# Kernel optimization log

Hardware: AMD Instinct MI355X
Metric: run time of the kernel (lower is better)

## Reference

```python
import jax, jax.numpy as jnp
import numpy as np

N = 20000          # nodes
E = 320000         # edges (avg degree 16)
F_IN = 512         # in_channels
HID = 64           # hidden_channels
H1 = 8             # conv1 heads (hard-coded in source)
C_OUT = 7          # out_channels (num classes)
OUT2 = C_OUT * C_OUT  # conv2 per-head output dim = out_channels**2
H2 = 8             # conv2 heads
NC = 64            # number of clusters
NIDX = 10000       # |cluster_index|
NEG_SLOPE = 0.2    # PyG GATConv default leaky-relu slope


def gat_conv(x, edge_index, W, att_src, att_dst, bias, concat):
    """PyG GATConv (add_self_loops=True, eval mode so attention dropout is off)."""
    n = x.shape[0]
    H, C = att_src.shape
    h = (x @ W).reshape(n, H, C)                      # [n, H, C]
    loop = jnp.arange(n)
    src = jnp.concatenate([edge_index[0], loop])      # self loops appended
    dst = jnp.concatenate([edge_index[1], loop])
    a_src = jnp.einsum('nhc,hc->nh', h, att_src)      # [n, H]
    a_dst = jnp.einsum('nhc,hc->nh', h, att_dst)
    e = jax.nn.leaky_relu(a_src[src] + a_dst[dst], NEG_SLOPE)   # [Etot, H]
    # segment softmax over incoming edges of each destination node
    m = jax.lax.stop_gradient(jax.ops.segment_max(e, dst, num_segments=n))
    p = jnp.exp(e - m[dst])
    denom = jax.ops.segment_sum(p, dst, num_segments=n)
    alpha = p / denom[dst]                            # [Etot, H]
    out = jax.ops.segment_sum(alpha[:, :, None] * h[src], dst, num_segments=n)  # [n, H, C]
    if concat:
        return out.reshape(n, H * C) + bias
    return out.mean(axis=1) + bias


def setup_inputs() -> dict:
    key = jax.random.key(0)
    ks = jax.random.split(key, 12)
    s1 = 1.0 / np.sqrt(F_IN)
    s2 = 1.0 / np.sqrt(2 * HID * H1)
    return {
        'x': jax.random.normal(ks[0], (N, F_IN), dtype=jnp.float32),
        'edge_index': jax.random.randint(ks[1], (2, E), 0, N),
        'cluster_id': jax.random.uniform(ks[2], (N, NC), dtype=jnp.float32),
        'cluster_index': jax.random.randint(ks[3], (NIDX,), 0, N),
        'W1': jax.random.normal(ks[4], (F_IN, H1 * HID), dtype=jnp.float32) * s1,
        'att_src1': jax.random.normal(ks[5], (H1, HID), dtype=jnp.float32) * 0.1,
        'att_dst1': jax.random.normal(ks[6], (H1, HID), dtype=jnp.float32) * 0.1,
        'b1': jnp.zeros((H1 * HID,), dtype=jnp.float32),
        'W2': jax.random.normal(ks[7], (2 * H1 * HID, H2 * OUT2), dtype=jnp.float32) * s2,
        'att_src2': jax.random.normal(ks[8], (H2, OUT2), dtype=jnp.float32) * 0.1,
        'att_dst2': jax.random.normal(ks[9], (H2, OUT2), dtype=jnp.float32) * 0.1,
        'b2': jnp.zeros((OUT2,), dtype=jnp.float32),
    }


def reference(x, edge_index, cluster_id, cluster_index,
              W1, att_src1, att_dst1, b1, W2, att_src2, att_dst2, b2):
    n = x.shape[0]
    # eval mode: F.dropout and attention dropout are identity
    h = jax.nn.elu(gat_conv(x, edge_index, W1, att_src1, att_dst1, b1, concat=True))  # [N, H1*HID]
    cid = cluster_id[cluster_index]                       # [NIDX, NC]
    cluster_features = (cid.T @ h[cluster_index]) / cid.sum(0)[:, None]  # [NC, H1*HID]
    x1 = cluster_features[jnp.argmax(cluster_id, axis=1)] # [N, H1*HID]
    xx = jnp.concatenate([jnp.concatenate([h, x1], 1),
                          jnp.concatenate([x1, h], 1)], 0)  # [2N, 2*H1*HID]
    ei2 = jnp.concatenate([edge_index, edge_index + n], 1)  # doubled graph
    return gat_conv(xx, ei2, W2, att_src2, att_dst2, b2, concat=False)  # [2N, OUT2]
```

## Files before the change

### kernel.cpp

```cpp
#include <hip/hip_runtime.h>

#define NNODES 20000
#define NEDGES 320000
#define FIN    512
#define HC1    512
#define NHEAD  8
#define OUT2   49
#define NCOL2  392
#define NB2    784
#define NCLU   64
#define NIDX   10000
#define NEG    0.2f

typedef unsigned short u16;
typedef short bf16x8 __attribute__((ext_vector_type(8)));
typedef float f32x4 __attribute__((ext_vector_type(4)));

static __device__ __forceinline__ float lrelu(float v){ return v > 0.f ? v : NEG*v; }

static __device__ __forceinline__ u16 f2bf_hi(float f, float& rem) {
  union { float f; unsigned u; } c; c.f = f;
  unsigned hb = c.u & 0xFFFF0000u;
  union { unsigned u; float f; } d; d.u = hb;
  rem = f - d.f;
  return (u16)(hb >> 16);
}
static __device__ __forceinline__ u16 f2bf(float f) {
  union { float f; unsigned u; } c; c.f = f;
  return (u16)(c.u >> 16);
}
static __device__ __forceinline__ u16 f2bf_rn(float f) {
  union { float f; unsigned u; } c; c.f = f;
  unsigned r = c.u + 0x7FFFu + ((c.u >> 16) & 1u);
  return (u16)(r >> 16);
}
static __device__ __forceinline__ float bf2f(u16 u) {
  union { unsigned u; float f; } c; c.u = ((unsigned)u) << 16;
  return c.f;
}
static __device__ __forceinline__ void load8bf(const u16* p, float* o) {
  ushort4 a = *(const ushort4*)p;
  ushort4 b = *(const ushort4*)(p + 4);
  o[0]=bf2f(a.x); o[1]=bf2f(a.y); o[2]=bf2f(a.z); o[3]=bf2f(a.w);
  o[4]=bf2f(b.x); o[5]=bf2f(b.y); o[6]=bf2f(b.z); o[7]=bf2f(b.w);
}

__global__ void tw1_kernel(const float* __restrict__ W1, u16* __restrict__ Th, u16* __restrict__ Tl) {
  int idx = blockIdx.x*256 + threadIdx.x;
  int k = idx >> 9, j = idx & 511;
  float rem; u16 hi = f2bf_hi(W1[idx], rem);
  Th[(size_t)j*512 + k] = hi;
  Tl[(size_t)j*512 + k] = f2bf(rem);
}

__global__ void tb2_kernel(const float* __restrict__ W2, u16* __restrict__ Th, u16* __restrict__ Tl) {
  int idx = blockIdx.x*256 + threadIdx.x;
  int k = idx / NB2, j = idx - k*NB2;
  float v = (j < NCOL2) ? W2[(size_t)k*NCOL2 + j] : W2[(size_t)(512+k)*NCOL2 + (j - NCOL2)];
  float rem; u16 hi = f2bf_hi(v, rem);
  Th[(size_t)j*512 + k] = hi;
  Tl[(size_t)j*512 + k] = f2bf(rem);
}

template<int EPI>
__global__ __launch_bounds__(256) void gemm_mfma(
    const float* __restrict__ A,
    const u16* __restrict__ Bh, const u16* __restrict__ Bl,
    u16* __restrict__ Cbf, int M, int Ncols,
    const int* __restrict__ cmax, const float* __restrict__ CFW, u16* __restrict__ h2)
{
  __shared__ __align__(16) u16 As[2][128][40];
  __shared__ __align__(16) u16 Bs[2][128][40];
  int tid = threadIdx.x;
  int row0 = blockIdx.x * 128;
  int col0 = blockIdx.y * 128;
  int lane = tid & 63;
  int wid = tid >> 6;
  int wr = (wid >> 1) * 64;
  int wc = (wid & 1) * 64;
  int l16 = lane & 15;
  int q = lane >> 4;
  f32x4 acc[4][4];
  #pragma unroll
  for (int i = 0; i < 4; i++)
    #pragma unroll
    for (int j = 0; j < 4; j++)
      acc[i][j] = (f32x4){0.f, 0.f, 0.f, 0.f};

  int srow = tid >> 2;
  int sq = tid & 3;
  const uint4 z4 = make_uint4(0,0,0,0);

  for (int k0 = 0; k0 < 512; k0 += 32) {
    #pragma unroll
    for (int part = 0; part < 2; part++) {
      int r = part*64 + srow;
      int gm = row0 + r;
      float4 v0 = make_float4(0.f,0.f,0.f,0.f), v1 = v0;
      if (gm < M) {
        v0 = *(const float4*)(A + (size_t)gm*512 + k0 + sq*8);
        v1 = *(const float4*)(A + (size_t)gm*512 + k0 + sq*8 + 4);
      }
      float rem;
      ushort4 h0, l0, h1, l1;
      h0.x = f2bf_hi(v0.x, rem); l0.x = f2bf(rem);
      h0.y = f2bf_hi(v0.y, rem); l0.y = f2bf(rem);
      h0.z = f2bf_hi(v0.z, rem); l0.z = f2bf(rem);
      h0.w = f2bf_hi(v0.w, rem); l0.w = f2bf(rem);
      h1.x = f2bf_hi(v1.x, rem); l1.x = f2bf(rem);
      h1.y = f2bf_hi(v1.y, rem); l1.y = f2bf(rem);
      h1.z = f2bf_hi(v1.z, rem); l1.z = f2bf(rem);
      h1.w = f2bf_hi(v1.w, rem); l1.w = f2bf(rem);
      *(ushort4*)&As[0][r][sq*8]     = h0;
      *(ushort4*)&As[0][r][sq*8 + 4] = h1;
      *(ushort4*)&As[1][r][sq*8]     = l0;
      *(ushort4*)&As[1][r][sq*8 + 4] = l1;
      int gn = col0 + r;
      uint4 wh = z4, wl = z4;
      if (gn < Ncols) {
        wh = *(const uint4*)(Bh + (size_t)gn*512 + k0 + sq*8);
        wl = *(const uint4*)(Bl + (size_t)gn*512 + k0 + sq*8);
      }
      *(uint4*)&Bs[0][r][sq*8] = wh;
      *(uint4*)&Bs[1][r][sq*8] = wl;
    }
    __syncthreads();
    bf16x8 ah[4], al[4], bh[4], bl[4];
    #pragma unroll
    for (int i = 0; i < 4; i++) {
      ah[i] = *(const bf16x8*)&As[0][wr + i*16 + l16][q*8];
      al[i] = *(const bf16x8*)&As[1][wr + i*16 + l16][q*8];
      bh[i] = *(const bf16x8*)&Bs[0][wc + i*16 + l16][q*8];
      bl[i] = *(const bf16x8*)&Bs[1][wc + i*16 + l16][q*8];
    }
    #pragma unroll
    for (int i = 0; i < 4; i++)
      #pragma unroll
      for (int j = 0; j < 4; j++) {
        acc[i][j] = __builtin_amdgcn_mfma_f32_16x16x32_bf16(ah[i], bh[j], acc[i][j], 0, 0, 0);
        acc[i][j] = __builtin_amdgcn_mfma_f32_16x16x32_bf16(ah[i], bl[j], acc[i][j], 0, 0, 0);
        acc[i][j] = __builtin_amdgcn_mfma_f32_16x16x32_bf16(al[i], bh[j], acc[i][j], 0, 0, 0);
      }
    __syncthreads();
  }

  if (EPI == 0) {
    #pragma unroll
    for (int i = 0; i < 4; i++) {
      #pragma unroll
      for (int r = 0; r < 4; r++) {
        int m = row0 + wr + i*16 + q*4 + r;
        if (m < M) {
          #pragma unroll
          for (int j = 0; j < 4; j++)
            Cbf[(size_t)m*Ncols + col0 + wc + j*16 + l16] = f2bf_rn(acc[i][j][r]);
        }
      }
    }
  } else {
    #pragma unroll
    for (int i = 0; i < 4; i++) {
      #pragma unroll
      for (int r = 0; r < 4; r++) {
        int m = row0 + wr + i*16 + q*4 + r;
        if (m >= M) continue;
        int c = cmax[m];
        const float* cf = CFW + (size_t)c * NB2;
        #pragma unroll
        for (int j = 0; j < 4; j++) {
          int n = col0 + wc + j*16 + l16;
          if (n >= NB2) continue;
          float v = acc[i][j][r];
          if (n < NCOL2) h2[(size_t)m*NCOL2 + n] = f2bf_rn(v + cf[NCOL2 + n]);
          else           h2[(size_t)(NNODES + m)*NCOL2 + (n - NCOL2)] = f2bf_rn(v + cf[n - NCOL2]);
        }
      }
    }
  }
}

__global__ void hist_kernel(const int* __restrict__ ei, int* __restrict__ counts) {
  int e = blockIdx.x*256 + threadIdx.x;
  if (e < NEDGES) atomicAdd(&counts[ei[NEDGES + e]], 1);
}

__global__ __launch_bounds__(1024) void scan_kernel(const int* __restrict__ counts,
                                                    int* __restrict__ rowptr, int* __restrict__ cursor) {
  __shared__ int part[1024];
  int t = threadIdx.x;
  const int CH = 20;
  int start = t*CH;
  int end = min(start+CH, NNODES);
  int sum = 0;
  for (int i = start; i < end; i++) sum += counts[i];
  part[t] = sum;
  __syncthreads();
  for (int off = 1; off < 1024; off <<= 1) {
    int v = part[t];
    int add = (t >= off) ? part[t-off] : 0;
    __syncthreads();
    part[t] = v + add;
    __syncthreads();
  }
  int run = part[t] - sum;
  for (int i = start; i < end; i++) {
    rowptr[i] = run; cursor[i] = run;
    run += counts[i];
  }
  if (t == 1023) rowptr[NNODES] = part[1023];
}

__global__ void scatter_kernel(const int* __restrict__ ei, int* __restrict__ cursor, int* __restrict__ csr) {
  int e = blockIdx.x*256 + threadIdx.x;
  if (e < NEDGES) {
    int src = ei[e];
    int dst = ei[NEDGES + e];
    int pos = atomicAdd(&cursor[dst], 1);
    csr[pos] = src;
  }
}

__global__ __launch_bounds__(256) void a1_kernel(
    const u16* __restrict__ hpre, const float* __restrict__ atts, const float* __restrict__ attd,
    float* __restrict__ as1, float* __restrict__ ad1)
{
  int lane = threadIdx.x & 63;
  int i = blockIdx.x*4 + (threadIdx.x >> 6);
  float hv[8];
  load8bf(hpre + (size_t)i*HC1 + lane*8, hv);
  const float* ap = atts + lane*8; const float* dp = attd + lane*8;
  float ps = 0.f, pd = 0.f;
  #pragma unroll
  for (int k = 0; k < 8; k++) { ps = fmaf(hv[k], ap[k], ps); pd = fmaf(hv[k], dp[k], pd); }
  ps += __shfl_down(ps, 4, 8); ps += __shfl_down(ps, 2, 8); ps += __shfl_down(ps, 1, 8);
  pd += __shfl_down(pd, 4, 8); pd += __shfl_down(pd, 2, 8); pd += __shfl_down(pd, 1, 8);
  if ((lane & 7) == 0) {
    as1[i*8 + (lane >> 3)] = ps;
    ad1[i*8 + (lane >> 3)] = pd;
  }
}

__global__ __launch_bounds__(256) void softmax1_kernel(
    const float* __restrict__ as1, const float* __restrict__ ad1,
    const int* __restrict__ rp, const int* __restrict__ csr,
    float* __restrict__ p1, float* __restrict__ selfw, float* __restrict__ invs)
{
  int gid = blockIdx.x*256 + threadIdx.x;
  int i = gid >> 3, h = gid & 7;
  int rs = rp[i], re = rp[i+1];
  float adst = ad1[gid];
  float ps = __expf(lrelu(as1[gid] + adst));
  float s = ps;
  for (int j = rs; j < re; j++) {
    float p = __expf(lrelu(as1[csr[j]*8 + h] + adst));
    p1[(size_t)j*8 + h] = p;
    s += p;
  }
  float inv = 1.f / s;
  selfw[gid] = ps * inv;
  invs[gid] = inv;
}

__global__ __launch_bounds__(256) void softmax2_kernel(
    const float* __restrict__ as2, const float* __restrict__ ad2,
    const int* __restrict__ rp, const int* __restrict__ csr,
    float* __restrict__ p2, float* __restrict__ selfw, float* __restrict__ invs)
{
  int gid = blockIdx.x*256 + threadIdx.x;
  int u = gid >> 3, h = gid & 7;
  int bn = (u < NNODES) ? u : u - NNODES;
  int off = u - bn;
  size_t eoff = (u < NNODES) ? 0 : NEDGES;
  int rs = rp[bn], re = rp[bn+1];
  float adst = ad2[gid];
  float ps = __expf(lrelu(as2[gid] + adst));
  float s = ps;
  for (int j = rs; j < re; j++) {
    float p = __expf(lrelu(as2[(csr[j]+off)*8 + h] + adst));
    p2[(eoff + (size_t)j)*8 + h] = p;
    s += p;
  }
  float inv = 1.f / s;
  selfw[gid] = ps * inv;
  invs[gid] = inv;
}

__global__ __launch_bounds__(256) void agg1_kernel(
    const u16* __restrict__ hpre, const float* __restrict__ p1,
    const float* __restrict__ selfw, const float* __restrict__ invs,
    const int* __restrict__ rowptr, const int* __restrict__ csr, const float* __restrict__ b1,
    float* __restrict__ hout)
{
  int lane = threadIdx.x & 63;
  int i = blockIdx.x*4 + (threadIdx.x >> 6);
  int hd = lane >> 3;
  int rs = rowptr[i];
  int deg = rowptr[i+1] - rs;
  float inv = invs[i*8 + hd];
  float asf = selfw[i*8 + hd];
  float acc[8];
  {
    float v[8];
    load8bf(hpre + (size_t)i*HC1 + lane*8, v);
    #pragma unroll
    for (int k = 0; k < 8; k++) acc[k] = asf * v[k];
  }
  int j = 0;
  for (; j + 1 < deg; j += 2) {
    int s0 = csr[rs+j], s1 = csr[rs+j+1];
    float al0 = p1[(size_t)(rs+j)*8 + hd] * inv;
    float al1 = p1[(size_t)(rs+j+1)*8 + hd] * inv;
    float v0[8], v1[8];
    load8bf(hpre + (size_t)s0*HC1 + lane*8, v0);
    load8bf(hpre + (size_t)s1*HC1 + lane*8, v1);
    #pragma unroll
    for (int k = 0; k < 8; k++) acc[k] = fmaf(al0, v0[k], acc[k]);
    #pragma unroll
    for (int k = 0; k < 8; k++) acc[k] = fmaf(al1, v1[k], acc[k]);
  }
  if (j < deg) {
    int s0 = csr[rs+j];
    float al0 = p1[(size_t)(rs+j)*8 + hd] * inv;
    float v0[8];
    load8bf(hpre + (size_t)s0*HC1 + lane*8, v0);
    #pragma unroll
    for (int k = 0; k < 8; k++) acc[k] = fmaf(al0, v0[k], acc[k]);
  }
  float o[8];
  #pragma unroll
  for (int k = 0; k < 8; k++) {
    float v = acc[k] + b1[lane*8 + k];
    o[k] = v > 0.f ? v : __expf(v) - 1.f;
  }
  float* ho = hout + (size_t)i*HC1 + lane*8;
  *(float4*)ho     = make_float4(o[0],o[1],o[2],o[3]);
  *(float4*)(ho+4) = make_float4(o[4],o[5],o[6],o[7]);
}

__global__ __launch_bounds__(256) void colsum_kernel(
    const float* __restrict__ cluster_id, const int* __restrict__ cidx, float* __restrict__ colsum)
{
  __shared__ float part[4][64];
  int tid = threadIdx.x; int q = tid >> 6, col = tid & 63;
  int start = blockIdx.x*313, end = min(start+313, NIDX);
  float acc = 0.f;
  for (int t = start + q; t < end; t += 4) {
    int node = cidx[t];
    acc += cluster_id[(size_t)node*NCLU + col];
  }
  part[q][col] = acc;
  __syncthreads();
  if (tid < 64) {
    float v = part[0][tid] + part[1][tid] + part[2][tid] + part[3][tid];
    atomicAdd(&colsum[tid], v);
  }
}

__global__ __launch_bounds__(256) void cf_kernel(
    const float* __restrict__ cluster_id, const int* __restrict__ cidx,
    const float* __restrict__ h, float* __restrict__ CFraw)
{
  int tid = threadIdx.x;
  int ch = blockIdx.y*64 + (tid & 63);
  int cb = blockIdx.x*16 + (tid >> 6)*4;
  int start = blockIdx.z*400, end = start + 400;
  float a0=0.f, a1=0.f, a2=0.f, a3=0.f;
  #pragma unroll 4
  for (int t = start; t < end; t++) {
    int node = cidx[t];
    float hv = h[(size_t)node*HC1 + ch];
    const float* cp = cluster_id + (size_t)node*NCLU + cb;
    a0 = fmaf(cp[0], hv, a0); a1 = fmaf(cp[1], hv, a1);
    a2 = fmaf(cp[2], hv, a2); a3 = fmaf(cp[3], hv, a3);
  }
  atomicAdd(&CFraw[(size_t)(cb+0)*HC1 + ch], a0);
  atomicAdd(&CFraw[(size_t)(cb+1)*HC1 + ch], a1);
  atomicAdd(&CFraw[(size_t)(cb+2)*HC1 + ch], a2);
  atomicAdd(&CFraw[(size_t)(cb+3)*HC1 + ch], a3);
}

__global__ __launch_bounds__(256) void argmax_kernel(const float* __restrict__ cluster_id, int* __restrict__ cmax)
{
  int lane = threadIdx.x & 63;
  int i = blockIdx.x*4 + (threadIdx.x >> 6);
  float v = cluster_id[(size_t)i*NCLU + lane];
  int idx = lane;
  #pragma unroll
  for (int off = 32; off > 0; off >>= 1) {
    float ov = __shfl_xor(v, off);
    int oi = __shfl_xor(idx, off);
    if (ov > v || (ov == v && oi < idx)) { v = ov; idx = oi; }
  }
  if (lane == 0) cmax[i] = idx;
}

__global__ __launch_bounds__(256) void cfw_kernel(
    const float* __restrict__ CFraw, const float* __restrict__ colsum,
    const float* __restrict__ W2, float* __restrict__ CFW)
{
  int o = blockIdx.x*256 + threadIdx.x;
  int c = o / NB2, j = o - c*NB2;
  const float* src = (j < NCOL2) ? (W2 + j) : (W2 + (size_t)512*NCOL2 + (j - NCOL2));
  float acc = 0.f;
  for (int k = 0; k < 512; k++) acc = fmaf(CFraw[(size_t)c*512 + k], src[(size_t)k*NCOL2], acc);
  CFW[o] = acc / colsum[c];
}

__global__ __launch_bounds__(256) void a2_kernel(
    const u16* __restrict__ h2, const float* __restrict__ atts, const float* __restrict__ attd,
    float* __restrict__ as2, float* __restrict__ ad2)
{
  __shared__ float rows[32*NCOL2];
  __shared__ float sa[NCOL2], sd[NCOL2];
  int tid = threadIdx.x;
  size_t base = (size_t)blockIdx.x * 32 * NCOL2;
  for (int idx = tid; idx < 32*NCOL2; idx += 256) rows[idx] = bf2f(h2[base + idx]);
  for (int idx = tid; idx < NCOL2; idx += 256) { sa[idx] = atts[idx]; sd[idx] = attd[idx]; }
  __syncthreads();
  int r = tid >> 3, hd = tid & 7;
  const float* rp = rows + r*NCOL2 + hd*OUT2;
  const float* ap = sa + hd*OUT2;
  const float* dp = sd + hd*OUT2;
  float ps = 0.f, pd = 0.f;
  #pragma unroll
  for (int j = 0; j < OUT2; j++) { float v = rp[j]; ps = fmaf(v, ap[j], ps); pd = fmaf(v, dp[j], pd); }
  int node = blockIdx.x*32 + r;
  as2[node*8 + hd] = ps;
  ad2[node*8 + hd] = pd;
}

__global__ __launch_bounds__(256) void agg2_kernel(
    const u16* __restrict__ h2, const float* __restrict__ p2,
    const float* __restrict__ selfw, const float* __restrict__ invs,
    const int* __restrict__ rowptr, const int* __restrict__ csr, const float* __restrict__ b2,
    float* __restrict__ out)
{
  __shared__ float red[4][NCOL2];
  int lane = threadIdx.x & 63;
  int w = threadIdx.x >> 6;
  int u = blockIdx.x*4 + w;
  int bn = (u < NNODES) ? u : u - NNODES;
  int off = u - bn;
  int rs = rowptr[bn];
  int deg = rowptr[bn+1] - rs;
  size_t pbase = (size_t)rs + (off ? NEDGES : 0);
  int hk[7]; float invk[7];
  #pragma unroll
  for (int k = 0; k < 7; k++) {
    int c = lane + 64*k;
    int hx = (c < NCOL2) ? (c / OUT2) : 0;
    hk[k] = hx;
    invk[k] = (c < NCOL2) ? invs[u*8 + hx] : 0.f;
  }
  float acc[7];
  {
    const u16* own = h2 + (size_t)u*NCOL2;
    #pragma unroll
    for (int k = 0; k < 7; k++) {
      int c = lane + 64*k;
      acc[k] = (c < NCOL2) ? selfw[u*8 + hk[k]] * bf2f(own[c]) : 0.f;
    }
  }
  int j = 0;
  for (; j + 1 < deg; j += 2) {
    int s0 = csr[rs+j] + off, s1 = csr[rs+j+1] + off;
    const float* pp0 = p2 + (pbase + j)*8;
    const float* pp1 = pp0 + 8;
    const u16* r0 = h2 + (size_t)s0*NCOL2;
    const u16* r1 = h2 + (size_t)s1*NCOL2;
    #pragma unroll
    for (int k = 0; k < 6; k++) {
      int c = lane + 64*k;
      acc[k] = fmaf(pp0[hk[k]]*invk[k], bf2f(r0[c]), acc[k]);
      acc[k] = fmaf(pp1[hk[k]]*invk[k], bf2f(r1[c]), acc[k]);
    }
    if (lane < 8) {
      int c = lane + 384;
      acc[6] = fmaf(pp0[hk[6]]*invk[6], bf2f(r0[c]), acc[6]);
      acc[6] = fmaf(pp1[hk[6]]*invk[6], bf2f(r1[c]), acc[6]);
    }
  }
  if (j < deg) {
    int s0 = csr[rs+j] + off;
    const float* pp0 = p2 + (pbase + j)*8;
    const u16* r0 = h2 + (size_t)s0*NCOL2;
    #pragma unroll
    for (int k = 0; k < 6; k++) {
      int c = lane + 64*k;
      acc[k] = fmaf(pp0[hk[k]]*invk[k], bf2f(r0[c]), acc[k]);
    }
    if (lane < 8) acc[6] = fmaf(pp0[hk[6]]*invk[6], bf2f(r0[lane+384]), acc[6]);
  }
  #pragma unroll
  for (int k = 0; k < 7; k++) { int c = lane + 64*k; if (c < NCOL2) red[w][c] = acc[k]; }
  __syncthreads();
  if (lane < OUT2) {
    float t = 0.f;
    #pragma unroll
    for (int h = 0; h < 8; h++) t += red[w][h*OUT2 + lane];
    out[(size_t)u*OUT2 + lane] = 0.125f*t + b2[lane];
  }
}

extern "C" void kernel_launch(void* const* d_in, const int* in_sizes, int n_in,
                              void* d_out, int out_size, void* d_ws, size_t ws_size,
                              hipStream_t stream)
{
  (void)in_sizes; (void)n_in; (void)out_size; (void)ws_size;
  const float* x     = (const float*)d_in[0];
  const int*   ei    = (const int*)d_in[1];
  const float* cid   = (const float*)d_in[2];
  const int*   cidx  = (const int*)d_in[3];
  const float* W1    = (const float*)d_in[4];
  const float* atts1 = (const float*)d_in[5];
  const float* attd1 = (const float*)d_in[6];
  const float* b1    = (const float*)d_in[7];
  const float* W2    = (const float*)d_in[8];
  const float* atts2 = (const float*)d_in[9];
  const float* attd2 = (const float*)d_in[10];
  const float* b2    = (const float*)d_in[11];
  float* out = (float*)d_out;

  char* ws = (char*)d_ws;
  size_t off = 0;
  auto alloc = [&](size_t b){ size_t r = off; off += (b + 255) & ~(size_t)255; return r; };
  size_t o_hpre = alloc((size_t)NNODES*HC1*2);
  size_t o_h    = alloc((size_t)NNODES*HC1*4);
  size_t o_h2   = alloc((size_t)2*NNODES*NCOL2*2);
  size_t o_w1h  = alloc((size_t)512*512*2);
  size_t o_w1l  = alloc((size_t)512*512*2);
  size_t o_b2h  = alloc((size_t)NB2*512*2);
  size_t o_b2l  = alloc((size_t)NB2*512*2);
  size_t o_CFW  = alloc((size_t)NCLU*NB2*4);
  size_t o_as1  = alloc((size_t)NNODES*8*4);
  size_t o_ad1  = alloc((size_t)NNODES*8*4);
  size_t o_as2  = alloc((size_t)2*NNODES*8*4);
  size_t o_ad2  = alloc((size_t)2*NNODES*8*4);
  size_t o_p1   = alloc((size_t)NEDGES*8*4);
  size_t o_p2   = alloc((size_t)2*NEDGES*8*4);
  size_t o_sw1  = alloc((size_t)NNODES*8*4);
  size_t o_iv1  = alloc((size_t)NNODES*8*4);
  size_t o_sw2  = alloc((size_t)2*NNODES*8*4);
  size_t o_iv2  = alloc((size_t)2*NNODES*8*4);
  size_t o_rp   = alloc((size_t)(NNODES+1)*4);
  size_t o_cur  = alloc((size_t)NNODES*4);
  size_t o_csr  = alloc((size_t)NEDGES*4);
  size_t o_cmax = alloc((size_t)NNODES*4);
  size_t o_cnt  = alloc((size_t)NNODES*4);
  size_t o_csum = alloc(256 + (size_t)NCLU*HC1*4);

  u16*   hpre  = (u16*)(ws + o_hpre);
  float* h     = (float*)(ws + o_h);
  u16*   h2    = (u16*)(ws + o_h2);
  u16*   w1h   = (u16*)(ws + o_w1h);
  u16*   w1l   = (u16*)(ws + o_w1l);
  u16*   b2h   = (u16*)(ws + o_b2h);
  u16*   b2l   = (u16*)(ws + o_b2l);
  float* CFW   = (float*)(ws + o_CFW);
  float* as1   = (float*)(ws + o_as1);
  float* ad1   = (float*)(ws + o_ad1);
  float* as2   = (float*)(ws + o_as2);
  float* ad2   = (float*)(ws + o_ad2);
  float* p1    = (float*)(ws + o_p1);
  float* p2    = (float*)(ws + o_p2);
  float* sw1   = (float*)(ws + o_sw1);
  float* iv1   = (float*)(ws + o_iv1);
  float* sw2   = (float*)(ws + o_sw2);
  float* iv2   = (float*)(ws + o_iv2);
  int*   rp    = (int*)(ws + o_rp);
  int*   cur   = (int*)(ws + o_cur);
  int*   csr   = (int*)(ws + o_csr);
  int*   cmax  = (int*)(ws + o_cmax);
  int*   cnt   = (int*)(ws + o_cnt);
  float* colsum= (float*)(ws + o_csum);
  float* CFraw = (float*)(ws + o_csum + 256);

  hipMemsetAsync(ws + o_cnt, 0, (size_t)NNODES*4, stream);
  hipMemsetAsync(ws + o_csum, 0, 256 + (size_t)NCLU*HC1*4, stream);

  tw1_kernel<<<1024, 256, 0, stream>>>(W1, w1h, w1l);
  tb2_kernel<<<1568, 256, 0, stream>>>(W2, b2h, b2l);
  hist_kernel<<<1250, 256, 0, stream>>>(ei, cnt);
  scan_kernel<<<1, 1024, 0, stream>>>(cnt, rp, cur);
  scatter_kernel<<<1250, 256, 0, stream>>>(ei, cur, csr);
  gemm_mfma<0><<<dim3(157,4), 256, 0, stream>>>(x, w1h, w1l, hpre, NNODES, 512, nullptr, nullptr, nullptr);
  a1_kernel<<<5000, 256, 0, stream>>>(hpre, atts1, attd1, as1, ad1);
  softmax1_kernel<<<625, 256, 0, stream>>>(as1, ad1, rp, csr, p1, sw1, iv1);
  agg1_kernel<<<5000, 256, 0, stream>>>(hpre, p1, sw1, iv1, rp, csr, b1, h);
  colsum_kernel<<<32, 256, 0, stream>>>(cid, cidx, colsum);
  cf_kernel<<<dim3(4,8,25), 256, 0, stream>>>(cid, cidx, h, CFraw);
  argmax_kernel<<<5000, 256, 0, stream>>>(cid, cmax);
  cfw_kernel<<<196, 256, 0, stream>>>(CFraw, colsum, W2, CFW);
  gemm_mfma<1><<<dim3(157,7), 256, 0, stream>>>(h, b2h, b2l, nullptr, NNODES, NB2, cmax, CFW, h2);
  a2_kernel<<<1250, 256, 0, stream>>>(h2, atts2, attd2, as2, ad2);
  softmax2_kernel<<<1250, 256, 0, stream>>>(as2, ad2, rp, csr, p2, sw2, iv2);
  agg2_kernel<<<10000, 256, 0, stream>>>(h2, p2, sw2, iv2, rp, csr, b2, out);
}
```

Baseline: 723.4 us.

## Pre-split GEMM operands into k-chunked bf16 hi/lo layout with direct-to-LDS loads

The fp32 activations are now split into bf16 hi/lo halves ahead of time. The input x gets a new split kernel, and agg1 writes h this way in its epilogue. Both are stored in a k-chunk-major layout (8 elements per chunk, rows padded to MPAD), and the weights are re-laid out the same way. The GEMM then loads tiles with global_load_lds, one wave per operand, which removes the in-loop fp32 conversion and register staging. This costs an extra pass over x and a strided layout for h that cf_kernel must now read and reconstruct. The MFMA issue order is also regrouped by product term.

```diff
diff --git a/kernel.cpp b/kernel.cpp
--- a/kernel.cpp
+++ b/kernel.cpp
@@ -1,6 +1,7 @@
 #include <hip/hip_runtime.h>
 
 #define NNODES 20000
+#define MPAD   20096
 #define NEDGES 320000
 #define FIN    512
 #define HC1    512
@@ -8,6 +9,7 @@
 #define OUT2   49
 #define NCOL2  392
 #define NB2    784
+#define NPAD2  896
 #define NCLU   64
 #define NIDX   10000
 #define NEG    0.2f
@@ -45,41 +47,99 @@
   o[4]=bf2f(b.x); o[5]=bf2f(b.y); o[6]=bf2f(b.z); o[7]=bf2f(b.w);
 }
 
+typedef __attribute__((address_space(3))) unsigned int lds_u32;
+typedef __attribute__((address_space(1))) const unsigned int glb_u32;
+static __device__ __forceinline__ void gl_lds16(const u16* g, u16* l) {
+  __builtin_amdgcn_global_load_lds((glb_u32*)g, (lds_u32*)l, 16, 0, 0);
+}
+
+__global__ void split4_kernel(const float* __restrict__ x, u16* __restrict__ xh, u16* __restrict__ xl) {
+  int tid = blockIdx.x*256 + threadIdx.x;
+  int i = tid >> 6;
+  int j = tid & 63;
+  const float* p = x + (size_t)i*FIN + j*8;
+  float4 v0 = *(const float4*)p, v1 = *(const float4*)(p+4);
+  float rem; ushort4 h0,h1,l0,l1;
+  h0.x = f2bf_hi(v0.x, rem); l0.x = f2bf(rem);
+  h0.y = f2bf_hi(v0.y, rem); l0.y = f2bf(rem);
+  h0.z = f2bf_hi(v0.z, rem); l0.z = f2bf(rem);
+  h0.w = f2bf_hi(v0.w, rem); l0.w = f2bf(rem);
+  h1.x = f2bf_hi(v1.x, rem); l1.x = f2bf(rem);
+  h1.y = f2bf_hi(v1.y, rem); l1.y = f2bf(rem);
+  h1.z = f2bf_hi(v1.z, rem); l1.z = f2bf(rem);
+  h1.w = f2bf_hi(v1.w, rem); l1.w = f2bf(rem);
+  size_t o = ((size_t)j*MPAD + i)*8;
+  *(ushort4*)&xh[o] = h0; *(ushort4*)&xh[o+4] = h1;
+  *(ushort4*)&xl[o] = l0; *(ushort4*)&xl[o+4] = l1;
+}
+
 __global__ void tw1_kernel(const float* __restrict__ W1, u16* __restrict__ Th, u16* __restrict__ Tl) {
-  int idx = blockIdx.x*256 + threadIdx.x;
-  int k = idx >> 9, j = idx & 511;
-  float rem; u16 hi = f2bf_hi(W1[idx], rem);
-  Th[(size_t)j*512 + k] = hi;
-  Tl[(size_t)j*512 + k] = f2bf(rem);
+  int tid = blockIdx.x*256 + threadIdx.x;
+  int kc = tid >> 9, j = tid & 511;
+  float rem; ushort4 h0,h1,l0,l1;
+  h0.x = f2bf_hi(W1[(size_t)(kc*8+0)*512 + j], rem); l0.x = f2bf(rem);
+  h0.y = f2bf_hi(W1[(size_t)(kc*8+1)*512 + j], rem); l0.y = f2bf(rem);
+  h0.z = f2bf_hi(W1[(size_t)(kc*8+2)*512 + j], rem); l0.z = f2bf(rem);
+  h0.w = f2bf_hi(W1[(size_t)(kc*8+3)*512 + j], rem); l0.w = f2bf(rem);
+  h1.x = f2bf_hi(W1[(size_t)(kc*8+4)*512 + j], rem); l1.x = f2bf(rem);
+  h1.y = f2bf_hi(W1[(size_t)(kc*8+5)*512 + j], rem); l1.y = f2bf(rem);
+  h1.z = f2bf_hi(W1[(size_t)(kc*8+6)*512 + j], rem); l1.z = f2bf(rem);
+  h1.w = f2bf_hi(W1[(size_t)(kc*8+7)*512 + j], rem); l1.w = f2bf(rem);
+  size_t o = ((size_t)kc*512 + j)*8;
+  *(ushort4*)&Th[o] = h0; *(ushort4*)&Th[o+4] = h1;
+  *(ushort4*)&Tl[o] = l0; *(ushort4*)&Tl[o+4] = l1;
 }
 
 __global__ void tb2_kernel(const float* __restrict__ W2, u16* __restrict__ Th, u16* __restrict__ Tl) {
-  int idx = blockIdx.x*256 + threadIdx.x;
-  int k = idx / NB2, j = idx - k*NB2;
-  float v = (j < NCOL2) ? W2[(size_t)k*NCOL2 + j] : W2[(size_t)(512+k)*NCOL2 + (j - NCOL2)];
-  float rem; u16 hi = f2bf_hi(v, rem);
-  Th[(size_t)j*512 + k] = hi;
-  Tl[(size_t)j*512 + k] = f2bf(rem);
+  int tid = blockIdx.x*256 + threadIdx.x;
+  int kc = tid / NPAD2, j = tid - kc*NPAD2;
+  float v[8];
+  #pragma unroll
+  for (int e = 0; e < 8; e++) {
+    int k = kc*8 + e;
+    v[e] = (j < NCOL2) ? W2[(size_t)k*NCOL2 + j]
+         : ((j < NB2) ? W2[(size_t)(512+k)*NCOL2 + (j - NCOL2)] : 0.f);
+  }
+  float rem; ushort4 h0,h1,l0,l1;
+  h0.x = f2bf_hi(v[0], rem); l0.x = f2bf(rem);
+  h0.y = f2bf_hi(v[1], rem); l0.y = f2bf(rem);
+  h0.z = f2bf_hi(v[2], rem); l0.z = f2bf(rem);
+  h0.w = f2bf_hi(v[3], rem); l0.w = f2bf(rem);
+  h1.x = f2bf_hi(v[4], rem); l1.x = f2bf(rem);
+  h1.y = f2bf_hi(v[5], rem); l1.y = f2bf(rem);
+  h1.z = f2bf_hi(v[6], rem); l1.z = f2bf(rem);
+  h1.w = f2bf_hi(v[7], rem); l1.w = f2bf(rem);
+  size_t o = ((size_t)kc*NPAD2 + j)*8;
+  *(ushort4*)&Th[o] = h0; *(ushort4*)&Th[o+4] = h1;
+  *(ushort4*)&Tl[o] = l0; *(ushort4*)&Tl[o+4] = l1;
 }
 
 template<int EPI>
 __global__ __launch_bounds__(256) void gemm_mfma(
-    const float* __restrict__ A,
+    const u16* __restrict__ Ah, const u16* __restrict__ Al,
     const u16* __restrict__ Bh, const u16* __restrict__ Bl,
+    int Apitch, int Bpitch,
     u16* __restrict__ Cbf, int M, int Ncols,
     const int* __restrict__ cmax, const float* __restrict__ CFW, u16* __restrict__ h2)
 {
-  __shared__ __align__(16) u16 As[2][128][40];
-  __shared__ __align__(16) u16 Bs[2][128][40];
+  __shared__ __align__(16) u16 S[16512];
   int tid = threadIdx.x;
+  int lane = tid & 63;
+  int w = tid >> 6;
   int row0 = blockIdx.x * 128;
   int col0 = blockIdx.y * 128;
-  int lane = tid & 63;
-  int wid = tid >> 6;
-  int wr = (wid >> 1) * 64;
-  int wc = (wid & 1) * 64;
+
+  const u16* G; size_t pitch; int lb;
+  if      (w == 0) { G = Ah + ((size_t)row0 + lane)*8; pitch = (size_t)Apitch; lb = 0; }
+  else if (w == 1) { G = Al + ((size_t)row0 + lane)*8; pitch = (size_t)Apitch; lb = 4128; }
+  else if (w == 2) { G = Bh + ((size_t)col0 + lane)*8; pitch = (size_t)Bpitch; lb = 8256; }
+  else             { G = Bl + ((size_t)col0 + lane)*8; pitch = (size_t)Bpitch; lb = 12384; }
+
+  int wr = (w >> 1) * 64;
+  int wc = (w & 1) * 64;
   int l16 = lane & 15;
   int q = lane >> 4;
+
   f32x4 acc[4][4];
   #pragma unroll
   for (int i = 0; i < 4; i++)
@@ -87,60 +147,39 @@
     for (int j = 0; j < 4; j++)
       acc[i][j] = (f32x4){0.f, 0.f, 0.f, 0.f};
 
-  int srow = tid >> 2;
-  int sq = tid & 3;
-  const uint4 z4 = make_uint4(0,0,0,0);
-
-  for (int k0 = 0; k0 < 512; k0 += 32) {
-    #pragma unroll
-    for (int part = 0; part < 2; part++) {
-      int r = part*64 + srow;
-      int gm = row0 + r;
-      float4 v0 = make_float4(0.f,0.f,0.f,0.f), v1 = v0;
-      if (gm < M) {
-        v0 = *(const float4*)(A + (size_t)gm*512 + k0 + sq*8);
-        v1 = *(const float4*)(A + (size_t)gm*512 + k0 + sq*8 + 4);
-      }
-      float rem;
-      ushort4 h0, l0, h1, l1;
-      h0.x = f2bf_hi(v0.x, rem); l0.x = f2bf(rem);
-      h0.y = f2bf_hi(v0.y, rem); l0.y = f2bf(rem);
-      h0.z = f2bf_hi(v0.z, rem); l0.z = f2bf(rem);
-      h0.w = f2bf_hi(v0.w, rem); l0.w = f2bf(rem);
-      h1.x = f2bf_hi(v1.x, rem); l1.x = f2bf(rem);
-      h1.y = f2bf_hi(v1.y, rem); l1.y = f2bf(rem);
-      h1.z = f2bf_hi(v1.z, rem); l1.z = f2bf(rem);
-      h1.w = f2bf_hi(v1.w, rem); l1.w = f2bf(rem);
-      *(ushort4*)&As[0][r][sq*8]     = h0;
-      *(ushort4*)&As[0][r][sq*8 + 4] = h1;
-      *(ushort4*)&As[1][r][sq*8]     = l0;
-      *(ushort4*)&As[1][r][sq*8 + 4] = l1;
-      int gn = col0 + r;
-      uint4 wh = z4, wl = z4;
-      if (gn < Ncols) {
-        wh = *(const uint4*)(Bh + (size_t)gn*512 + k0 + sq*8);
-        wl = *(const uint4*)(Bl + (size_t)gn*512 + k0 + sq*8);
-      }
-      *(uint4*)&Bs[0][r][sq*8] = wh;
-      *(uint4*)&Bs[1][r][sq*8] = wl;
+  for (int t = 0; t < 16; t++) {
+    #pragma unroll
+    for (int c = 0; c < 4; c++) {
+      const u16* g = G + ((size_t)(t*4 + c))*pitch*8;
+      gl_lds16(g,       &S[lb + c*1032]);
+      gl_lds16(g + 512, &S[lb + c*1032 + 512]);
     }
     __syncthreads();
     bf16x8 ah[4], al[4], bh[4], bl[4];
     #pragma unroll
     for (int i = 0; i < 4; i++) {
-      ah[i] = *(const bf16x8*)&As[0][wr + i*16 + l16][q*8];
-      al[i] = *(const bf16x8*)&As[1][wr + i*16 + l16][q*8];
-      bh[i] = *(const bf16x8*)&Bs[0][wc + i*16 + l16][q*8];
-      bl[i] = *(const bf16x8*)&Bs[1][wc + i*16 + l16][q*8];
+      int ra = q*1032 + (wr + i*16 + l16)*8;
+      int rb = q*1032 + (wc + i*16 + l16)*8;
+      ah[i] = *(const bf16x8*)&S[ra];
+      al[i] = *(const bf16x8*)&S[4128 + ra];
+      bh[i] = *(const bf16x8*)&S[8256 + rb];
+      bl[i] = *(const bf16x8*)&S[12384 + rb];
     }
     #pragma unroll
     for (int i = 0; i < 4; i++)
       #pragma unroll
-      for (int j = 0; j < 4; j++) {
+      for (int j = 0; j < 4; j++)
         acc[i][j] = __builtin_amdgcn_mfma_f32_16x16x32_bf16(ah[i], bh[j], acc[i][j], 0, 0, 0);
+    #pragma unroll
+    for (int i = 0; i < 4; i++)
+      #pragma unroll
+      for (int j = 0; j < 4; j++)
         acc[i][j] = __builtin_amdgcn_mfma_f32_16x16x32_bf16(ah[i], bl[j], acc[i][j], 0, 0, 0);
+    #pragma unroll
+    for (int i = 0; i < 4; i++)
+      #pragma unroll
+      for (int j = 0; j < 4; j++)
         acc[i][j] = __builtin_amdgcn_mfma_f32_16x16x32_bf16(al[i], bh[j], acc[i][j], 0, 0, 0);
-      }
     __syncthreads();
   }
 
@@ -289,7 +328,7 @@
     const u16* __restrict__ hpre, const float* __restrict__ p1,
     const float* __restrict__ selfw, const float* __restrict__ invs,
     const int* __restrict__ rowptr, const int* __restrict__ csr, const float* __restrict__ b1,
-    float* __restrict__ hout)
+    u16* __restrict__ hh, u16* __restrict__ hl)
 {
   int lane = threadIdx.x & 63;
   int i = blockIdx.x*4 + (threadIdx.x >> 6);
@@ -326,15 +365,24 @@
     #pragma unroll
     for (int k = 0; k < 8; k++) acc[k] = fmaf(al0, v0[k], acc[k]);
   }
+  float rem; ushort4 h0,h1,l0,l1;
   float o[8];
   #pragma unroll
   for (int k = 0; k < 8; k++) {
     float v = acc[k] + b1[lane*8 + k];
     o[k] = v > 0.f ? v : __expf(v) - 1.f;
   }
-  float* ho = hout + (size_t)i*HC1 + lane*8;
-  *(float4*)ho     = make_float4(o[0],o[1],o[2],o[3]);
-  *(float4*)(ho+4) = make_float4(o[4],o[5],o[6],o[7]);
+  h0.x = f2bf_hi(o[0], rem); l0.x = f2bf(rem);
+  h0.y = f2bf_hi(o[1], rem); l0.y = f2bf(rem);
+  h0.z = f2bf_hi(o[2], rem); l0.z = f2bf(rem);
+  h0.w = f2bf_hi(o[3], rem); l0.w = f2bf(rem);
+  h1.x = f2bf_hi(o[4], rem); l1.x = f2bf(rem);
+  h1.y = f2bf_hi(o[5], rem); l1.y = f2bf(rem);
+  h1.z = f2bf_hi(o[6], rem); l1.z = f2bf(rem);
+  h1.w = f2bf_hi(o[7], rem); l1.w = f2bf(rem);
+  size_t o16 = ((size_t)lane*MPAD + i)*8;
+  *(ushort4*)&hh[o16] = h0; *(ushort4*)&hh[o16+4] = h1;
+  *(ushort4*)&hl[o16] = l0; *(ushort4*)&hl[o16+4] = l1;
 }
 
 __global__ __launch_bounds__(256) void colsum_kernel(
@@ -358,17 +406,19 @@
 
 __global__ __launch_bounds__(256) void cf_kernel(
     const float* __restrict__ cluster_id, const int* __restrict__ cidx,
-    const float* __restrict__ h, float* __restrict__ CFraw)
+    const u16* __restrict__ hh, const u16* __restrict__ hl, float* __restrict__ CFraw)
 {
   int tid = threadIdx.x;
   int ch = blockIdx.y*64 + (tid & 63);
   int cb = blockIdx.x*16 + (tid >> 6)*4;
   int start = blockIdx.z*400, end = start + 400;
+  size_t choff = ((size_t)(ch >> 3)*MPAD)*8 + (ch & 7);
   float a0=0.f, a1=0.f, a2=0.f, a3=0.f;
   #pragma unroll 4
   for (int t = start; t < end; t++) {
     int node = cidx[t];
-    float hv = h[(size_t)node*HC1 + ch];
+    size_t idx = choff + (size_t)node*8;
+    float hv = bf2f(hh[idx]) + bf2f(hl[idx]);
     const float* cp = cluster_id + (size_t)node*NCLU + cb;
     a0 = fmaf(cp[0], hv, a0); a1 = fmaf(cp[1], hv, a1);
     a2 = fmaf(cp[2], hv, a2); a3 = fmaf(cp[3], hv, a3);
@@ -525,12 +575,15 @@
   size_t off = 0;
   auto alloc = [&](size_t b){ size_t r = off; off += (b + 255) & ~(size_t)255; return r; };
   size_t o_hpre = alloc((size_t)NNODES*HC1*2);
-  size_t o_h    = alloc((size_t)NNODES*HC1*4);
   size_t o_h2   = alloc((size_t)2*NNODES*NCOL2*2);
-  size_t o_w1h  = alloc((size_t)512*512*2);
-  size_t o_w1l  = alloc((size_t)512*512*2);
-  size_t o_b2h  = alloc((size_t)NB2*512*2);
-  size_t o_b2l  = alloc((size_t)NB2*512*2);
+  size_t o_xh   = alloc((size_t)64*MPAD*8*2);
+  size_t o_xl   = alloc((size_t)64*MPAD*8*2);
+  size_t o_hh   = alloc((size_t)64*MPAD*8*2);
+  size_t o_hl   = alloc((size_t)64*MPAD*8*2);
+  size_t o_w1h  = alloc((size_t)64*512*8*2);
+  size_t o_w1l  = alloc((size_t)64*512*8*2);
+  size_t o_b2h  = alloc((size_t)64*NPAD2*8*2);
+  size_t o_b2l  = alloc((size_t)64*NPAD2*8*2);
   size_t o_CFW  = alloc((size_t)NCLU*NB2*4);
   size_t o_as1  = alloc((size_t)NNODES*8*4);
   size_t o_ad1  = alloc((size_t)NNODES*8*4);
@@ -550,8 +603,11 @@
   size_t o_csum = alloc(256 + (size_t)NCLU*HC1*4);
 
   u16*   hpre  = (u16*)(ws + o_hpre);
-  float* h     = (float*)(ws + o_h);
   u16*   h2    = (u16*)(ws + o_h2);
+  u16*   xh    = (u16*)(ws + o_xh);
+  u16*   xl    = (u16*)(ws + o_xl);
+  u16*   hh    = (u16*)(ws + o_hh);
+  u16*   hl    = (u16*)(ws + o_hl);
   u16*   w1h   = (u16*)(ws + o_w1h);
   u16*   w1l   = (u16*)(ws + o_w1l);
   u16*   b2h   = (u16*)(ws + o_b2h);
@@ -578,20 +634,21 @@
   hipMemsetAsync(ws + o_cnt, 0, (size_t)NNODES*4, stream);
   hipMemsetAsync(ws + o_csum, 0, 256 + (size_t)NCLU*HC1*4, stream);
 
-  tw1_kernel<<<1024, 256, 0, stream>>>(W1, w1h, w1l);
-  tb2_kernel<<<1568, 256, 0, stream>>>(W2, b2h, b2l);
+  split4_kernel<<<5000, 256, 0, stream>>>(x, xh, xl);
+  tw1_kernel<<<128, 256, 0, stream>>>(W1, w1h, w1l);
+  tb2_kernel<<<224, 256, 0, stream>>>(W2, b2h, b2l);
   hist_kernel<<<1250, 256, 0, stream>>>(ei, cnt);
   scan_kernel<<<1, 1024, 0, stream>>>(cnt, rp, cur);
   scatter_kernel<<<1250, 256, 0, stream>>>(ei, cur, csr);
-  gemm_mfma<0><<<dim3(157,4), 256, 0, stream>>>(x, w1h, w1l, hpre, NNODES, 512, nullptr, nullptr, nullptr);
+  gemm_mfma<0><<<dim3(157,4), 256, 0, stream>>>(xh, xl, w1h, w1l, MPAD, 512, hpre, NNODES, 512, nullptr, nullptr, nullptr);
   a1_kernel<<<5000, 256, 0, stream>>>(hpre, atts1, attd1, as1, ad1);
   softmax1_kernel<<<625, 256, 0, stream>>>(as1, ad1, rp, csr, p1, sw1, iv1);
-  agg1_kernel<<<5000, 256, 0, stream>>>(hpre, p1, sw1, iv1, rp, csr, b1, h);
+  agg1_kernel<<<5000, 256, 0, stream>>>(hpre, p1, sw1, iv1, rp, csr, b1, hh, hl);
   colsum_kernel<<<32, 256, 0, stream>>>(cid, cidx, colsum);
-  cf_kernel<<<dim3(4,8,25), 256, 0, stream>>>(cid, cidx, h, CFraw);
+  cf_kernel<<<dim3(4,8,25), 256, 0, stream>>>(cid, cidx, hh, hl, CFraw);
   argmax_kernel<<<5000, 256, 0, stream>>>(cid, cmax);
   cfw_kernel<<<196, 256, 0, stream>>>(CFraw, colsum, W2, CFW);
-  gemm_mfma<1><<<dim3(157,7), 256, 0, stream>>>(h, b2h, b2l, nullptr, NNODES, NB2, cmax, CFW, h2);
+  gemm_mfma<1><<<dim3(157,7), 256, 0, stream>>>(hh, hl, b2h, b2l, MPAD, NPAD2, nullptr, NNODES, NB2, cmax, CFW, h2);
   a2_kernel<<<1250, 256, 0, stream>>>(h2, atts2, attd2, as2, ad2);
   softmax2_kernel<<<1250, 256, 0, stream>>>(as2, ad2, rp, csr, p2, sw2, iv2);
   agg2_kernel<<<10000, 256, 0, stream>>>(h2, p2, sw2, iv2, rp, csr, b2, out);
```

After: 793.6 us. 9.7% more time.
